# Kernel optimization log

Hardware: AMD Instinct MI355X
Metric: run time of the kernel (lower is better)

The kernel has to match this reference:

```python
import jax, jax.numpy as jnp
import numpy as np

# Shapes: n groups, l = max group length, d = d_h, N = total queries (nq.sum()).
N_Q, N_GRP, L, D = 4096, 256, 64, 512


def setup_inputs() -> dict:
    key = jax.random.key(0)
    ks = jax.random.split(key, 8)
    q = jax.random.normal(ks[0], (N_Q, 2 * D), dtype=jnp.float32)      # cat([h_src, h_dst])
    k = jax.random.normal(ks[1], (N_GRP, L, D), dtype=jnp.float32)      # h_grp
    v = jax.random.normal(ks[2], (N_GRP, L, D), dtype=jnp.float32)      # x_grp
    m = (jax.random.uniform(ks[3], (N_GRP, L)) > 0.2).astype(jnp.float32)
    # sorted group id per query == repeat_interleave(arange(n), nq)
    gid = jnp.sort(jax.random.randint(ks[4], (N_Q,), 0, N_GRP))
    Wq = jax.random.normal(ks[5], (2 * D, D), dtype=jnp.float32) / np.float32(np.sqrt(2 * D))
    bq = jnp.zeros((D,), dtype=jnp.float32)
    Wk = jax.random.normal(ks[6], (D, D), dtype=jnp.float32) / np.float32(np.sqrt(D))
    bk = jnp.zeros((D,), dtype=jnp.float32)
    return dict(q=q, k=k, v=v, m=m, gid=gid, Wq=Wq, bq=bq, Wk=Wk, bk=bk)


def reference(q, k, v, m, gid, Wq, bq, Wk, bk):
    """Faithful jax version of NounPhraseModel.attention.

    torch: q -> self.q(q); k -> self.k(k); repeat_interleave(nq, 0) on k/v/m;
    s = (k @ q) / sqrt(d) - (exp(50*(1-m)) - 1); out = (v * softmax(s, 1)).sum(1).
    repeat_interleave is expressed as a gather by the per-query group id `gid`.
    """
    d = k.shape[-1]
    qp = q @ Wq + bq                                   # (N, d)   self.q(q)
    kp = k @ Wk + bk                                   # (n, l, d) self.k(k)
    kg = kp[gid]                                       # (N, l, d)
    vg = v[gid]                                        # (N, l, d)
    mg = m[gid]                                        # (N, l)
    s = jnp.einsum('nd,nld->nl', qp, kg) / jnp.sqrt(jnp.float32(d))
    s = s - (jnp.exp(50.0 * (1.0 - mg)) - 1.0)         # exponential mask bias
    a = jax.nn.softmax(s, axis=1)                      # softmax over group length
    return jnp.einsum('nl,nld->nd', a, vg)             # (N, d)
```

## Files before the change

### kernel.cpp

```cpp
#include <hip/hip_runtime.h>

#define NQ   4096
#define NGRP 256
#define LL   64
#define DD   512

typedef __attribute__((ext_vector_type(8))) short short8v;
typedef __attribute__((ext_vector_type(4))) float f32x4;
typedef __attribute__((ext_vector_type(4))) unsigned short us4v;

#define SCALE 0.044194173824159216f

static __device__ __forceinline__ unsigned short f2bf(float f) {
  union { float f; unsigned u; } x{f};
  unsigned r = x.u + 0x7fffu + ((x.u >> 16) & 1u);
  return (unsigned short)(r >> 16);
}
static __device__ __forceinline__ float bf2f(unsigned short h) {
  union { unsigned u; float f; } x{(unsigned)h << 16};
  return x.f;
}

static __device__ __forceinline__ void gload16(const void* g, void* lds_wave_base) {
  __builtin_amdgcn_global_load_lds(
      (const __attribute__((address_space(1))) void*)g,
      (__attribute__((address_space(3))) void*)lds_wave_base, 16, 0, 0);
}

static __device__ __forceinline__ uint4 pack8(float4 f0, float4 f1) {
  uint4 pk;
  pk.x = (unsigned)f2bf(f0.x) | ((unsigned)f2bf(f0.y) << 16);
  pk.y = (unsigned)f2bf(f0.z) | ((unsigned)f2bf(f0.w) << 16);
  pk.z = (unsigned)f2bf(f1.x) | ((unsigned)f2bf(f1.y) << 16);
  pk.w = (unsigned)f2bf(f1.z) | ((unsigned)f2bf(f1.w) << 16);
  return pk;
}

static __device__ __forceinline__ void split_store(
    unsigned short* Hh, unsigned short* Hl, int r, int c4, float4 v) {
  int s = c4 >> 1, hf = c4 & 1;
  int base = (r * 8 + (s ^ (r & 7))) * 8 + hf * 4;
  unsigned short h0 = f2bf(v.x), h1 = f2bf(v.y), h2 = f2bf(v.z), h3 = f2bf(v.w);
  us4v hv = {h0, h1, h2, h3};
  us4v lv = {f2bf(v.x - bf2f(h0)), f2bf(v.y - bf2f(h1)),
             f2bf(v.z - bf2f(h2)), f2bf(v.w - bf2f(h3))};
  *(us4v*)(Hh + base) = hv;
  *(us4v*)(Hl + base) = lv;
}

static __device__ __forceinline__ short8v frag(const unsigned short* P, int r, int sl) {
  return *(const short8v*)(P + (r * 8 + (sl ^ (r & 7))) * 8);
}
static __device__ __forceinline__ short8v frag16(const unsigned short* P, int r, int sl) {
  return *(const short8v*)(P + (r * 16 + (sl ^ (r & 7))) * 8);
}

__global__ __launch_bounds__(256) void k_prep(
    const float* __restrict__ q_in, const float* __restrict__ k_in,
    const int* __restrict__ gid,
    const float* __restrict__ Wk, const float* __restrict__ Wq,
    const float* __restrict__ bq,
    unsigned short* __restrict__ qbf, unsigned short* __restrict__ kbf,
    int* __restrict__ starts,
    float* __restrict__ b2, unsigned short* __restrict__ w2t) {
  __shared__ __align__(16) unsigned short lds[4 * 64 * 64];
  int b = blockIdx.x, t = threadIdx.x;
  if (b < 128) {
    unsigned short* Ah = lds;
    unsigned short* Al = lds + 4096;
    unsigned short* Bh = lds + 8192;
    unsigned short* Bl = lds + 12288;
    int lane = t & 63, wid = t >> 6;
    int wm = wid >> 1, wn = wid & 1;
    int n0 = (b & 15) * 64, m0 = (b >> 4) * 64;
    f32x4 acc[2][2];
    #pragma unroll
    for (int i = 0; i < 2; ++i)
      #pragma unroll
      for (int j = 0; j < 2; ++j) acc[i][j] = (f32x4){0.f,0.f,0.f,0.f};

    for (int k0 = 0; k0 < 512; k0 += 64) {
      __syncthreads();
      #pragma unroll
      for (int i = 0; i < 4; ++i) {
        int idx = i * 256 + t, r = idx >> 4, c4 = idx & 15;
        float4 vA = *(const float4*)&Wk[(size_t)(m0 + r) * 512 + k0 + c4 * 4];
        split_store(Ah, Al, r, c4, vA);
        float4 vB = *(const float4*)&Wq[(size_t)(n0 + r) * 512 + k0 + c4 * 4];
        split_store(Bh, Bl, r, c4, vB);
      }
      __syncthreads();
      #pragma unroll
      for (int kk = 0; kk < 2; ++kk) {
        int sl = kk * 4 + (lane >> 4);
        short8v aH[2], aL[2], bH[2], bL[2];
        #pragma unroll
        for (int fm = 0; fm < 2; ++fm) {
          int r = wm * 32 + fm * 16 + (lane & 15);
          aH[fm] = frag(Ah, r, sl); aL[fm] = frag(Al, r, sl);
        }
        #pragma unroll
        for (int fn = 0; fn < 2; ++fn) {
          int r = wn * 32 + fn * 16 + (lane & 15);
          bH[fn] = frag(Bh, r, sl); bL[fn] = frag(Bl, r, sl);
        }
        #pragma unroll
        for (int fm = 0; fm < 2; ++fm)
          #pragma unroll
          for (int fn = 0; fn < 2; ++fn) {
            acc[fm][fn] = __builtin_amdgcn_mfma_f32_16x16x32_bf16(aH[fm], bH[fn], acc[fm][fn], 0, 0, 0);
            acc[fm][fn] = __builtin_amdgcn_mfma_f32_16x16x32_bf16(aH[fm], bL[fn], acc[fm][fn], 0, 0, 0);
            acc[fm][fn] = __builtin_amdgcn_mfma_f32_16x16x32_bf16(aL[fm], bH[fn], acc[fm][fn], 0, 0, 0);
          }
      }
    }
    int cn = lane & 15, rq = lane >> 4;
    #pragma unroll
    for (int fm = 0; fm < 2; ++fm)
      #pragma unroll
      for (int fn = 0; fn < 2; ++fn)
        #pragma unroll
        for (int j = 0; j < 4; ++j) {
          int m = m0 + wm * 32 + fm * 16 + rq * 4 + j;
          int n = n0 + wn * 32 + fn * 16 + cn;
          w2t[(size_t)m * 1024 + n] = f2bf(acc[fm][fn][j]);
        }
  } else if (b < 2176) {
    int idx = (b - 128) * 256 + t;
    const float* src = q_in + (size_t)idx * 8;
    ((uint4*)qbf)[idx] = pack8(*(const float4*)src, *(const float4*)(src + 4));
  } else if (b == 2176) {
    for (int g = t; g <= NGRP; g += 256) {
      int lo = 0, hi = NQ;
      while (lo < hi) { int mid = (lo + hi) >> 1; if (gid[mid] < g) lo = mid + 1; else hi = mid; }
      starts[g] = lo;
    }
  } else if (b < 2179) {
    int dd = (b - 2177) * 256 + t;
    if (dd < DD) {
      float s = 0.f;
      const float* row = Wk + (size_t)dd * DD;
      for (int j = 0; j < DD; j += 4) {
        float4 w = *(const float4*)&row[j];
        float4 bb = *(const float4*)&bq[j];
        s += w.x*bb.x + w.y*bb.y + w.z*bb.z + w.w*bb.w;
      }
      b2[dd] = s;
    }
  } else {
    int idx = (b - 2179) * 256 + t;
    const float* src = k_in + (size_t)idx * 8;
    ((uint4*)kbf)[idx] = pack8(*(const float4*)src, *(const float4*)(src + 4));
  }
}

__global__ __launch_bounds__(256) void gemm_qt_mfma(
    const unsigned short* __restrict__ qbf,
    const unsigned short* __restrict__ w2t,
    const float* __restrict__ b2,
    unsigned short* __restrict__ qt) {
  __shared__ __align__(16) unsigned short As[64 * 128];
  __shared__ __align__(16) unsigned short Bs[64 * 128];
  int t = threadIdx.x;
  int lane = t & 63, wid = t >> 6;
  int wm = wid >> 1, wn = wid & 1;
  int n0 = blockIdx.x * 64, m0 = blockIdx.y * 64;

  f32x4 acc[2][2];
  #pragma unroll
  for (int i = 0; i < 2; ++i)
    #pragma unroll
    for (int j = 0; j < 2; ++j) acc[i][j] = (f32x4){0.f, 0.f, 0.f, 0.f};

  for (int k0 = 0; k0 < 1024; k0 += 128) {
    __syncthreads();
    #pragma unroll
    for (int i = 0; i < 4; ++i) {
      int idx = i * 256 + t;
      int r = idx >> 4, ssw = idx & 15;
      int scol = ssw ^ (r & 7);
      gload16(qbf + (size_t)(m0 + r) * 1024 + k0 + scol * 8,
              (char*)As + (i * 256 + wid * 64) * 16);
      gload16(w2t + (size_t)(n0 + r) * 1024 + k0 + scol * 8,
              (char*)Bs + (i * 256 + wid * 64) * 16);
    }
    __syncthreads();
    #pragma unroll
    for (int kk = 0; kk < 4; ++kk) {
      short8v aF[2], bF[2];
      int sl = kk * 4 + (lane >> 4);
      #pragma unroll
      for (int fm = 0; fm < 2; ++fm)
        aF[fm] = frag16(As, wm * 32 + fm * 16 + (lane & 15), sl);
      #pragma unroll
      for (int fn = 0; fn < 2; ++fn)
        bF[fn] = frag16(Bs, wn * 32 + fn * 16 + (lane & 15), sl);
      #pragma unroll
      for (int fm = 0; fm < 2; ++fm)
        #pragma unroll
        for (int fn = 0; fn < 2; ++fn)
          acc[fm][fn] = __builtin_amdgcn_mfma_f32_16x16x32_bf16(aF[fm], bF[fn], acc[fm][fn], 0, 0, 0);
    }
  }
  int cn = lane & 15, rq = lane >> 4;
  #pragma unroll
  for (int fn = 0; fn < 2; ++fn) {
    int n = n0 + wn * 32 + fn * 16 + cn;
    float bias = b2[n];
    #pragma unroll
    for (int fm = 0; fm < 2; ++fm)
      #pragma unroll
      for (int j = 0; j < 4; ++j) {
        int m = m0 + wm * 32 + fm * 16 + rq * 4 + j;
        qt[(size_t)m * 512 + n] = f2bf(acc[fm][fn][j] + bias);
      }
  }
}

__global__ __launch_bounds__(256) void k_scores4(
    const unsigned short* __restrict__ qt,
    const unsigned short* __restrict__ kbf, const int* __restrict__ starts,
    float* __restrict__ s_part) {
  int g = blockIdx.x >> 2, dq = blockIdx.x & 3;
  int t = threadIdx.x, lane = t & 63, wl = t >> 6;
  int s0 = starts[g], s1 = starts[g + 1];
  if (s0 >= s1) return;

  __shared__ __align__(16) unsigned short Ks[64*64];
  __shared__ __align__(16) unsigned short Qs[32*64];

  float* sp = s_part + (size_t)dq * NQ * LL;

  for (int cs = s0; cs < s1; cs += 32) {
    int qc = min(32, s1 - cs);
    f32x4 acc[2];
    acc[0] = (f32x4){0.f,0.f,0.f,0.f};
    acc[1] = (f32x4){0.f,0.f,0.f,0.f};

    #pragma unroll
    for (int kt = 0; kt < 2; ++kt) {
      int k0 = dq * 128 + kt * 64;
      __syncthreads();
      #pragma unroll
      for (int i = 0; i < 2; ++i) {
        int idx = i * 256 + t;
        int r = idx >> 3, ssw = idx & 7;
        int scol = ssw ^ (r & 7);
        gload16(kbf + ((size_t)g * LL + r) * DD + k0 + scol * 8,
                (char*)Ks + (i * 256 + wl * 64) * 16);
      }
      {
        int r = t >> 3, ssw = t & 7;
        int scol = ssw ^ (r & 7);
        gload16(qt + (size_t)(cs + r) * DD + k0 + scol * 8,
                (char*)Qs + wl * 64 * 16);
      }
      __syncthreads();
      #pragma unroll
      for (int kk = 0; kk < 2; ++kk) {
        int sl = kk * 4 + (lane >> 4);
        short8v aF = frag(Ks, wl * 16 + (lane & 15), sl);
        #pragma unroll
        for (int fn = 0; fn < 2; ++fn) {
          short8v bF = frag(Qs, fn * 16 + (lane & 15), sl);
          acc[fn] = __builtin_amdgcn_mfma_f32_16x16x32_bf16(aF, bF, acc[fn], 0, 0, 0);
        }
      }
    }
    {
      int cq = lane & 15, rq = lane >> 4;
      #pragma unroll
      for (int fn = 0; fn < 2; ++fn) {
        int q = fn * 16 + cq;
        if (q < qc) {
          float* row = sp + (size_t)(cs + q) * LL;
          #pragma unroll
          for (int j = 0; j < 4; ++j)
            row[wl * 16 + rq * 4 + j] = acc[fn][j];
        }
      }
    }
  }
}

__global__ __launch_bounds__(256) void k_pv2(
    const float* __restrict__ s_part, const float* __restrict__ vv_,
    const float* __restrict__ msk, const int* __restrict__ starts,
    float* __restrict__ out) {
  int g = blockIdx.x >> 1, dh = blockIdx.x & 1;
  int t = threadIdx.x, lane = t & 63, wid = t >> 6;
  int s0 = starts[g], s1 = starts[g + 1];
  if (s0 >= s1) return;

  __shared__ __align__(16) float S_lds[32][68];
  __shared__ float bias_lds[LL];
  if (t < LL) bias_lds[t] = __expf(50.0f * (1.0f - msk[g * LL + t])) - 1.0f;

  const float* vb = vv_ + (size_t)g * LL * DD + dh * 256 + lane * 4;

  for (int cs = s0; cs < s1; cs += 32) {
    int qc = min(32, s1 - cs);
    __syncthreads();
    #pragma unroll
    for (int i = 0; i < 2; ++i) {
      int f = i * 256 + t;
      int q = f >> 4, l4 = f & 15;
      const float* p = s_part + (size_t)(cs + q) * LL + l4 * 4;
      float4 a0 = *(const float4*)p;
      float4 a1 = *(const float4*)(p + (size_t)NQ * LL);
      float4 a2 = *(const float4*)(p + (size_t)2 * NQ * LL);
      float4 a3 = *(const float4*)(p + (size_t)3 * NQ * LL);
      float4 r;
      r.x = (a0.x + a1.x + a2.x + a3.x) * SCALE - bias_lds[l4 * 4 + 0];
      r.y = (a0.y + a1.y + a2.y + a3.y) * SCALE - bias_lds[l4 * 4 + 1];
      r.z = (a0.z + a1.z + a2.z + a3.z) * SCALE - bias_lds[l4 * 4 + 2];
      r.w = (a0.w + a1.w + a2.w + a3.w) * SCALE - bias_lds[l4 * 4 + 3];
      *(float4*)&S_lds[q][l4 * 4] = r;
    }
    __syncthreads();
    {
      int q = t >> 3, i = t & 7;
      float4 x0 = *(const float4*)&S_lds[q][i * 8];
      float4 x1 = *(const float4*)&S_lds[q][i * 8 + 4];
      float mx = fmaxf(fmaxf(fmaxf(x0.x, x0.y), fmaxf(x0.z, x0.w)),
                       fmaxf(fmaxf(x1.x, x1.y), fmaxf(x1.z, x1.w)));
      #pragma unroll
      for (int off = 1; off < 8; off <<= 1) mx = fmaxf(mx, __shfl_xor(mx, off, 8));
      float e0 = __expf(x0.x - mx), e1 = __expf(x0.y - mx);
      float e2 = __expf(x0.z - mx), e3 = __expf(x0.w - mx);
      float e4 = __expf(x1.x - mx), e5 = __expf(x1.y - mx);
      float e6 = __expf(x1.z - mx), e7 = __expf(x1.w - mx);
      float sum = ((e0 + e1) + (e2 + e3)) + ((e4 + e5) + (e6 + e7));
      #pragma unroll
      for (int off = 1; off < 8; off <<= 1) sum += __shfl_xor(sum, off, 8);
      float inv = 1.0f / sum;
      *(float4*)&S_lds[q][i * 8]     = make_float4(e0 * inv, e1 * inv, e2 * inv, e3 * inv);
      *(float4*)&S_lds[q][i * 8 + 4] = make_float4(e4 * inv, e5 * inv, e6 * inv, e7 * inv);
    }
    __syncthreads();
    {
      float o[8][4];
      #pragma unroll
      for (int u = 0; u < 8; ++u)
        #pragma unroll
        for (int e = 0; e < 4; ++e) o[u][e] = 0.f;
      for (int l0 = 0; l0 < LL; l0 += 4) {
        float a_[8][4];
        #pragma unroll
        for (int u = 0; u < 8; ++u) {
          float4 av = *(const float4*)&S_lds[wid * 8 + u][l0];
          a_[u][0] = av.x; a_[u][1] = av.y; a_[u][2] = av.z; a_[u][3] = av.w;
        }
        #pragma unroll
        for (int e = 0; e < 4; ++e) {
          float4 vv = *(const float4*)&vb[(size_t)(l0 + e) * DD];
          #pragma unroll
          for (int u = 0; u < 8; ++u) {
            o[u][0] += a_[u][e] * vv.x;
            o[u][1] += a_[u][e] * vv.y;
            o[u][2] += a_[u][e] * vv.z;
            o[u][3] += a_[u][e] * vv.w;
          }
        }
      }
      #pragma unroll
      for (int u = 0; u < 8; ++u) {
        int q = wid * 8 + u;
        if (q < qc) {
          *(float4*)&out[(size_t)(cs + q) * DD + dh * 256 + lane * 4] =
              make_float4(o[u][0], o[u][1], o[u][2], o[u][3]);
        }
      }
    }
  }
}

extern "C" void kernel_launch(void* const* d_in, const int* in_sizes, int n_in,
                              void* d_out, int out_size, void* d_ws, size_t ws_size,
                              hipStream_t stream) {
  const float* q_in = (const float*)d_in[0];
  const float* k_in = (const float*)d_in[1];
  const float* v_in = (const float*)d_in[2];
  const float* m_in = (const float*)d_in[3];
  const int*   gid  = (const int*)d_in[4];
  const float* Wq   = (const float*)d_in[5];
  const float* bq   = (const float*)d_in[6];
  const float* Wk   = (const float*)d_in[7];
  float* out = (float*)d_out;

  unsigned short* w2t = (unsigned short*)d_ws;
  unsigned short* qt  = w2t + 512 * 1024;
  unsigned short* qbf = qt + 4096 * 512;
  float* b2 = (float*)(qbf + 4096 * 1024);
  int* starts = (int*)(b2 + 512);
  float* s_part = (float*)(starts + 512);
  unsigned short* kbf = (unsigned short*)(s_part + 4 * NQ * LL);

  k_prep<<<6275, 256, 0, stream>>>(q_in, k_in, gid, Wk, Wq, bq,
                                   qbf, kbf, starts, b2, w2t);
  gemm_qt_mfma<<<dim3(8, 64), 256, 0, stream>>>(qbf, w2t, b2, qt);
  k_scores4<<<NGRP * 4, 256, 0, stream>>>(qt, kbf, starts, s_part);
  k_pv2<<<NGRP * 2, 256, 0, stream>>>(s_part, v_in, m_in, starts, out);
}
```

Before: 64.13 us.

## Move K bf16 packing into GEMM launch and remap block IDs across XCDs

The K-to-bf16 conversion blocks move out of the prep kernel and are appended to the Q-projection GEMM launch as extra blocks, so that memory-bound conversion can overlap with the compute-bound GEMM and the prep kernel shrinks. The GEMM, scores and PV kernels also remap blockIdx so that consecutive logical blocks (same group or neighbouring tiles) land on the same XCD, aiming for better L2 reuse on the MI355X's chiplet layout. The risk is that the appended conversion blocks delay the GEMM tail, and the remapping depends on round-robin dispatch across 8 XCDs.

```diff
diff --git a/kernel.cpp b/kernel.cpp
--- a/kernel.cpp
+++ b/kernel.cpp
@@ -56,12 +56,10 @@
 }
 
 __global__ __launch_bounds__(256) void k_prep(
-    const float* __restrict__ q_in, const float* __restrict__ k_in,
-    const int* __restrict__ gid,
+    const float* __restrict__ q_in, const int* __restrict__ gid,
     const float* __restrict__ Wk, const float* __restrict__ Wq,
     const float* __restrict__ bq,
-    unsigned short* __restrict__ qbf, unsigned short* __restrict__ kbf,
-    int* __restrict__ starts,
+    unsigned short* __restrict__ qbf, int* __restrict__ starts,
     float* __restrict__ b2, unsigned short* __restrict__ w2t) {
   __shared__ __align__(16) unsigned short lds[4 * 64 * 64];
   int b = blockIdx.x, t = threadIdx.x;
@@ -135,7 +133,7 @@
       while (lo < hi) { int mid = (lo + hi) >> 1; if (gid[mid] < g) lo = mid + 1; else hi = mid; }
       starts[g] = lo;
     }
-  } else if (b < 2179) {
+  } else {
     int dd = (b - 2177) * 256 + t;
     if (dd < DD) {
       float s = 0.f;
@@ -147,10 +145,6 @@
       }
       b2[dd] = s;
     }
-  } else {
-    int idx = (b - 2179) * 256 + t;
-    const float* src = k_in + (size_t)idx * 8;
-    ((uint4*)kbf)[idx] = pack8(*(const float4*)src, *(const float4*)(src + 4));
   }
 }
 
@@ -158,13 +152,23 @@
     const unsigned short* __restrict__ qbf,
     const unsigned short* __restrict__ w2t,
     const float* __restrict__ b2,
-    unsigned short* __restrict__ qt) {
+    unsigned short* __restrict__ qt,
+    const float* __restrict__ k_in, unsigned short* __restrict__ kbf) {
   __shared__ __align__(16) unsigned short As[64 * 128];
   __shared__ __align__(16) unsigned short Bs[64 * 128];
-  int t = threadIdx.x;
+  int b = blockIdx.x, t = threadIdx.x;
+
+  if (b >= 512) {
+    int idx = (b - 512) * 256 + t;
+    const float* src = k_in + (size_t)idx * 8;
+    ((uint4*)kbf)[idx] = pack8(*(const float4*)src, *(const float4*)(src + 4));
+    return;
+  }
+
+  int logical = (b & 7) * 64 + (b >> 3);
+  int n0 = (logical & 7) * 64, m0 = (logical >> 3) * 64;
   int lane = t & 63, wid = t >> 6;
   int wm = wid >> 1, wn = wid & 1;
-  int n0 = blockIdx.x * 64, m0 = blockIdx.y * 64;
 
   f32x4 acc[2][2];
   #pragma unroll
@@ -221,7 +225,9 @@
     const unsigned short* __restrict__ qt,
     const unsigned short* __restrict__ kbf, const int* __restrict__ starts,
     float* __restrict__ s_part) {
-  int g = blockIdx.x >> 2, dq = blockIdx.x & 3;
+  int h = blockIdx.x;
+  int logical = (h & 7) * 128 + (h >> 3);
+  int g = logical >> 2, dq = logical & 3;
   int t = threadIdx.x, lane = t & 63, wl = t >> 6;
   int s0 = starts[g], s1 = starts[g + 1];
   if (s0 >= s1) return;
@@ -287,7 +293,9 @@
     const float* __restrict__ s_part, const float* __restrict__ vv_,
     const float* __restrict__ msk, const int* __restrict__ starts,
     float* __restrict__ out) {
-  int g = blockIdx.x >> 1, dh = blockIdx.x & 1;
+  int h = blockIdx.x;
+  int logical = (h & 7) * 64 + (h >> 3);
+  int g = logical >> 1, dh = logical & 1;
   int t = threadIdx.x, lane = t & 63, wid = t >> 6;
   int s0 = starts[g], s1 = starts[g + 1];
   if (s0 >= s1) return;
@@ -396,9 +404,8 @@
   float* s_part = (float*)(starts + 512);
   unsigned short* kbf = (unsigned short*)(s_part + 4 * NQ * LL);
 
-  k_prep<<<6275, 256, 0, stream>>>(q_in, k_in, gid, Wk, Wq, bq,
-                                   qbf, kbf, starts, b2, w2t);
-  gemm_qt_mfma<<<dim3(8, 64), 256, 0, stream>>>(qbf, w2t, b2, qt);
+  k_prep<<<2179, 256, 0, stream>>>(q_in, gid, Wk, Wq, bq, qbf, starts, b2, w2t);
+  gemm_qt_mfma<<<4608, 256, 0, stream>>>(qbf, w2t, b2, qt, k_in, kbf);
   k_scores4<<<NGRP * 4, 256, 0, stream>>>(qt, kbf, starts, s_part);
   k_pv2<<<NGRP * 2, 256, 0, stream>>>(s_part, v_in, m_in, starts, out);
 }
```

New measurement: 60.39 us. 5.8% less time.
